# Kernel tuning notes

Hardware: AMD Instinct MI355X
Metric: run time of the kernel (lower is better)

## Reference

```python
import jax, jax.numpy as jnp
import numpy as np
from jax import lax

# Static problem configuration (SAModule(ratio=0.25, r=0.2, MLP([35,64,64,128])))
B, N, C_IN = 8, 4096, 32
RATIO, R, K = 0.25, 0.2, 64   # K == max_num_neighbors
M = int(N * RATIO)            # centroids per cloud after FPS
NEG = -1e10


def setup_inputs() -> dict:
    key = jax.random.key(0)
    ks = jax.random.split(key, 6)
    x = jax.random.normal(ks[0], (B * N, C_IN), jnp.float32)
    pos = jax.random.uniform(ks[1], (B * N, 3), jnp.float32)  # unit cube -> r=0.2 balls are non-trivial
    batch = jnp.repeat(jnp.arange(B, dtype=jnp.int32), N)
    def lin(k, fan_in, fan_out):
        return jax.random.normal(k, (fan_in, fan_out), jnp.float32) * (1.0 / np.sqrt(fan_in))
    W1 = lin(ks[2], C_IN + 3, 64); b1 = jnp.zeros((64,), jnp.float32)
    W2 = lin(ks[3], 64, 64);       b2 = jnp.zeros((64,), jnp.float32)
    W3 = lin(ks[4], 64, 128);      b3 = jnp.zeros((128,), jnp.float32)
    return {"x": x, "pos": pos, "batch": batch,
            "W1": W1, "b1": b1, "W2": W2, "b2": b2, "W3": W3, "b3": b3}


def _fps_one(p):
    """Farthest-point sampling on one cloud p:[N,3] -> idx:[M] (deterministic start at 0)."""
    def body(carry, _):
        dmin, last = carry
        d = jnp.sum((p - p[last]) ** 2, axis=-1)         # [N] sq-dist to last picked point
        dmin = jnp.minimum(dmin, d)
        nxt = jnp.argmax(dmin).astype(jnp.int32)
        return (dmin, nxt), nxt
    init = (jnp.full((N,), 1e10, jnp.float32), jnp.int32(0))
    _, rest = lax.scan(body, init, None, length=M - 1)
    return jnp.concatenate([jnp.zeros((1,), jnp.int32), rest])


def _sa_one(p, xb, ib, W1, b1, W2, b2, W3, b3):
    """Radius ball-query + PointNetConv (gather -> MLP -> masked scatter-max) on one cloud."""
    ctr = p[ib]                                              # [M,3] sampled centroids
    d2 = jnp.sum((ctr[:, None, :] - p[None, :, :]) ** 2, -1)  # [M,N]
    negd, nbr = lax.top_k(-d2, K)                            # K nearest per centroid
    valid = (-negd) <= R * R                                 # inside-ball mask [M,K]
    xj = xb[nbr]                                             # [M,K,C_IN] gathered features
    rel = p[nbr] - ctr[:, None, :]                           # [M,K,3] relative positions
    h = jnp.concatenate([xj, rel], axis=-1)                  # message input [x_j, pos_j - pos_i]
    h = jax.nn.relu(h @ W1 + b1)
    h = jax.nn.relu(h @ W2 + b2)
    h = h @ W3 + b3                                          # plain last layer (PyG MLP plain_last)
    h = jnp.where(valid[..., None], h, NEG)
    return jnp.max(h, axis=1)                                # max aggregation -> [M,128]


def reference(x, pos, batch, W1, b1, W2, b2, W3, b3):
    pos3 = pos.reshape(B, N, 3)
    x3 = x.reshape(B, N, C_IN)
    idx = jax.vmap(_fps_one)(pos3)                           # [B,M]
    conv = lambda p, xb, ib: _sa_one(p, xb, ib, W1, b1, W2, b2, W3, b3)
    x_out = jax.vmap(conv)(pos3, x3, idx)                    # [B,M,128]
    pos_out = jnp.take_along_axis(pos3, idx[..., None], axis=1)  # [B,M,3]
    batch_out = jnp.repeat(jnp.arange(B, dtype=batch.dtype), M)
    return x_out.reshape(B * M, -1), pos_out.reshape(B * M, 3), batch_out
```

## Files before the change

kernel.cpp:

```cpp
#include <hip/hip_runtime.h>
#include <hip/hip_bf16.h>

#define BB 8
#define NN 4096
#define CIN 32
#define MM 1024
#define KNB 64
#define CAND 1024
#define ROWS 72
#define GRID 256
#define NWORK (GRID - 8)

typedef __attribute__((ext_vector_type(8))) short  short8;
typedef __attribute__((ext_vector_type(4))) float  f32x4;
typedef __attribute__((ext_vector_type(2))) float  f32x2;

__device__ __forceinline__ float sq3(float dx, float dy, float dz) {
    return __fadd_rn(__fadd_rn(__fmul_rn(dx, dx), __fmul_rn(dy, dy)), __fmul_rn(dz, dz));
}

__device__ __forceinline__ unsigned short f2bf(float v) {
    union { __hip_bfloat16 b; unsigned short u; } cv;
    cv.b = __float2bfloat16(v);
    return cv.u;
}
__device__ __forceinline__ float bf2f(unsigned short u) {
    union { unsigned short u; __hip_bfloat16 b; } cv;
    cv.u = u;
    return __bfloat162float(cv.b);
}

static __device__ __forceinline__ f32x4 mfma16(short8 a, short8 b, f32x4 c) {
    return __builtin_amdgcn_mfma_f32_16x16x32_bf16(a, b, c, 0, 0, 0);
}

template<int CTRL>
__device__ __forceinline__ unsigned long long dpp_maxkey(unsigned long long k) {
    unsigned int lo = (unsigned int)k;
    unsigned int hi = (unsigned int)(k >> 32);
    unsigned int nlo = (unsigned int)__builtin_amdgcn_update_dpp((int)lo, (int)lo, CTRL, 0xF, 0xF, false);
    unsigned int nhi = (unsigned int)__builtin_amdgcn_update_dpp((int)hi, (int)hi, CTRL, 0xF, 0xF, false);
    unsigned long long nk = ((unsigned long long)nhi << 32) | (unsigned long long)nlo;
    return nk > k ? nk : k;
}

__global__ __launch_bounds__(256) void prep_kernel(
    const float* __restrict__ W1, const float* __restrict__ W2,
    const float* __restrict__ W3, unsigned short* __restrict__ wf)
{
    int gid = blockIdx.x * 256 + threadIdx.x;
    const float* W; int K, Ncol, base, slot;
    if (gid < 1024)      { W = W1; K = 35; Ncol = 64;  base = 0;     slot = gid; }
    else if (gid < 2048) { W = W2; K = 64; Ncol = 64;  base = 8192;  slot = gid - 1024; }
    else                 { W = W3; K = 64; Ncol = 128; base = 16384; slot = gid - 2048; }
    int lane = slot & 63, h = (slot >> 6) & 1, kstep = (slot >> 7) & 1, tile = slot >> 8;
    int col = tile * 16 + (lane & 15), quad = lane >> 4;
#pragma unroll
    for (int j = 0; j < 8; ++j) {
        int k = kstep * 32 + quad * 8 + j;
        float wv = (k < K) ? W[k * Ncol + col] : 0.0f;
        unsigned short hi = f2bf(wv);
        unsigned short v = h ? f2bf(wv - bf2f(hi)) : hi;
        wf[base + slot * 8 + j] = v;
    }
}

struct SaShared {
    unsigned short HA[2 * 64 * ROWS];
    unsigned long long candk[CAND];
    int   cnt;
    int   ok;
    int   sel[KNB];
    float red[4][128];
};

__device__ __forceinline__ void sa_process(
    SaShared& sh, const float* __restrict__ x, const float* __restrict__ P,
    const unsigned short* __restrict__ wf,
    const float* __restrict__ b1, const float* __restrict__ b2,
    const float* __restrict__ b3, float* __restrict__ out, int bm, int b, int ci)
{
    const int t    = threadIdx.x;
    const int w    = t >> 6;
    const int lane = t & 63;
    const float R2 = (float)(0.2 * 0.2);

    if (t == 0) sh.cnt = 0;
    __syncthreads();

    const float cx = P[3 * ci], cy = P[3 * ci + 1], cz = P[3 * ci + 2];

    for (int i = t; i < NN; i += 256) {
        float dx = P[3 * i] - cx, dy = P[3 * i + 1] - cy, dz = P[3 * i + 2] - cz;
        float d2 = sq3(dx, dy, dz);
        bool hit = d2 <= R2;
        unsigned long long mk = __ballot(hit);
        if (mk) {
            int leader = __ffsll((unsigned long long)mk) - 1;
            int base = 0;
            if (lane == leader) base = atomicAdd(&sh.cnt, __popcll(mk));
            base = __shfl(base, leader);
            if (hit) {
                int p = base + __popcll(mk & ((1ull << lane) - 1));
                if (p < CAND)
                    sh.candk[p] = ((unsigned long long)__float_as_uint(d2) << 32)
                                | (unsigned int)i;
            }
        }
    }
    __syncthreads();
    const int n = min(sh.cnt, CAND);
    const int V = min(n, KNB);

    for (int i = t; i < n; i += 256) {
        unsigned long long ki = sh.candk[i];
        int rank = 0;
        for (int j = 0; j < n; ++j)
            rank += (sh.candk[j] < ki) ? 1 : 0;
        if (rank < KNB) sh.sel[rank] = (int)(ki & 0xffffffffu);
    }
    __syncthreads();

    {
        const int row = 16 * w + (lane & 15);
        const int prt = lane >> 4;
        short8 z = {};
        *(short8*)(sh.HA + row * ROWS + 32 + prt * 8) = z;
        *(short8*)(sh.HA + 64 * ROWS + row * ROWS + 32 + prt * 8) = z;
        if (row < V) {
            int g = b * NN + sh.sel[row];
            const float4* xr = (const float4*)(x + (size_t)g * CIN + prt * 8);
            float4 v0 = xr[0], v1 = xr[1];
            float vv[8] = {v0.x, v0.y, v0.z, v0.w, v1.x, v1.y, v1.z, v1.w};
            short8 hv, lv;
#pragma unroll
            for (int j = 0; j < 8; ++j) {
                unsigned short h = f2bf(vv[j]);
                hv[j] = (short)h;
                lv[j] = (short)f2bf(vv[j] - bf2f(h));
            }
            *(short8*)(sh.HA + row * ROWS + prt * 8) = hv;
            *(short8*)(sh.HA + 64 * ROWS + row * ROWS + prt * 8) = lv;
            if (prt == 0) {
                int g2 = sh.sel[row];
#pragma unroll
                for (int c = 0; c < 3; ++c) {
                    float cc = (c == 0) ? cx : (c == 1) ? cy : cz;
                    float rv = P[3 * g2 + c] - cc;
                    unsigned short h = f2bf(rv);
                    sh.HA[row * ROWS + 32 + c] = h;
                    sh.HA[64 * ROWS + row * ROWS + 32 + c] = f2bf(rv - bf2f(h));
                }
            }
        }
    }

    const int m16  = lane & 15;
    const int quad = lane >> 4;
    const int arow = 16 * w + m16;
    const short8* wf8 = (const short8*)wf;

    {
        short8 aH[2], aL[2];
        aH[0] = *(const short8*)(sh.HA + arow * ROWS + quad * 8);
        aH[1] = *(const short8*)(sh.HA + arow * ROWS + 32 + quad * 8);
        aL[0] = *(const short8*)(sh.HA + 64 * ROWS + arow * ROWS + quad * 8);
        aL[1] = *(const short8*)(sh.HA + 64 * ROWS + arow * ROWS + 32 + quad * 8);
#pragma unroll
        for (int tile = 0; tile < 4; ++tile) {
            f32x4 acc = {};
#pragma unroll
            for (int ks = 0; ks < 2; ++ks) {
                short8 bH = wf8[((tile * 2 + ks) * 2 + 0) * 64 + lane];
                short8 bL = wf8[((tile * 2 + ks) * 2 + 1) * 64 + lane];
                acc = mfma16(aH[ks], bH, acc);
                acc = mfma16(aH[ks], bL, acc);
                acc = mfma16(aL[ks], bH, acc);
            }
            int col = tile * 16 + m16;
            float bb = b1[col];
#pragma unroll
            for (int i = 0; i < 4; ++i) {
                int grow = 16 * w + quad * 4 + i;
                float v = fmaxf(acc[i] + bb, 0.0f);
                unsigned short h = f2bf(v);
                sh.HA[grow * ROWS + col] = h;
                sh.HA[64 * ROWS + grow * ROWS + col] = f2bf(v - bf2f(h));
            }
        }
    }

    {
        short8 aH[2], aL[2];
        aH[0] = *(const short8*)(sh.HA + arow * ROWS + quad * 8);
        aH[1] = *(const short8*)(sh.HA + arow * ROWS + 32 + quad * 8);
        aL[0] = *(const short8*)(sh.HA + 64 * ROWS + arow * ROWS + quad * 8);
        aL[1] = *(const short8*)(sh.HA + 64 * ROWS + arow * ROWS + 32 + quad * 8);
#pragma unroll
        for (int tile = 0; tile < 4; ++tile) {
            f32x4 acc = {};
#pragma unroll
            for (int ks = 0; ks < 2; ++ks) {
                short8 bH = wf8[1024 + ((tile * 2 + ks) * 2 + 0) * 64 + lane];
                short8 bL = wf8[1024 + ((tile * 2 + ks) * 2 + 1) * 64 + lane];
                acc = mfma16(aH[ks], bH, acc);
                acc = mfma16(aH[ks], bL, acc);
                acc = mfma16(aL[ks], bH, acc);
            }
            int col = tile * 16 + m16;
            float bb = b2[col];
#pragma unroll
            for (int i = 0; i < 4; ++i) {
                int grow = 16 * w + quad * 4 + i;
                float v = fmaxf(acc[i] + bb, 0.0f);
                unsigned short h = f2bf(v);
                sh.HA[grow * ROWS + col] = h;
                sh.HA[64 * ROWS + grow * ROWS + col] = f2bf(v - bf2f(h));
            }
        }
    }

    {
        short8 aH[2], aL[2];
        aH[0] = *(const short8*)(sh.HA + arow * ROWS + quad * 8);
        aH[1] = *(const short8*)(sh.HA + arow * ROWS + 32 + quad * 8);
        aL[0] = *(const short8*)(sh.HA + 64 * ROWS + arow * ROWS + quad * 8);
        aL[1] = *(const short8*)(sh.HA + 64 * ROWS + arow * ROWS + 32 + quad * 8);
#pragma unroll
        for (int tile = 0; tile < 8; ++tile) {
            f32x4 acc = {};
#pragma unroll
            for (int ks = 0; ks < 2; ++ks) {
                short8 bH = wf8[2048 + ((tile * 2 + ks) * 2 + 0) * 64 + lane];
                short8 bL = wf8[2048 + ((tile * 2 + ks) * 2 + 1) * 64 + lane];
                acc = mfma16(aH[ks], bH, acc);
                acc = mfma16(aH[ks], bL, acc);
                acc = mfma16(aL[ks], bH, acc);
            }
            float mv = -1e10f;
#pragma unroll
            for (int i = 0; i < 4; ++i) {
                int grow = 16 * w + quad * 4 + i;
                float v = (grow < V) ? acc[i] : -1e10f;
                mv = fmaxf(mv, v);
            }
            mv = fmaxf(mv, __shfl_xor(mv, 16));
            mv = fmaxf(mv, __shfl_xor(mv, 32));
            if (lane < 16) sh.red[w][tile * 16 + lane] = mv;
        }
    }
    __syncthreads();

    if (t < 128) {
        float v = fmaxf(fmaxf(sh.red[0][t], sh.red[1][t]),
                        fmaxf(sh.red[2][t], sh.red[3][t]));
        out[(size_t)bm * 128 + t] = v + b3[t];
    }
}

union SharedMem {
    struct {
        float4 plds4[NN];
        int    chosen[MM];
        __align__(16) unsigned long long part[2][4];
    } fps;
    SaShared sa;
};

__global__ __launch_bounds__(256, 2) void fused_kernel(
    const float* __restrict__ x, const float* __restrict__ pos,
    int* __restrict__ idx_ws, unsigned int* __restrict__ ready,
    int* __restrict__ done, const unsigned short* __restrict__ wf,
    const float* __restrict__ b1, const float* __restrict__ b2,
    const float* __restrict__ b3, float* __restrict__ out)
{
    __shared__ SharedMem sh;
    const int t = threadIdx.x;

    if (blockIdx.x < BB) {
        __builtin_amdgcn_s_setprio(3);
        const int b = blockIdx.x;
        const float* P = pos + (size_t)b * NN * 3;
        for (int i = t; i < NN; i += 256) {
            float4 v;
            v.x = P[3 * i]; v.y = P[3 * i + 1]; v.z = P[3 * i + 2]; v.w = 0.0f;
            sh.fps.plds4[i] = v;
        }
        if (t == 0) {
            sh.fps.chosen[0] = 0;
            __hip_atomic_store(&idx_ws[b * MM], 0, __ATOMIC_RELAXED,
                               __HIP_MEMORY_SCOPE_AGENT);
        }
        __syncthreads();

        f32x2 pxv[8], pyv[8], pzv[8], dminv[8];
#pragma unroll
        for (int s = 0; s < 8; ++s) {
            float4 a = sh.fps.plds4[t + 512 * s];
            float4 c = sh.fps.plds4[t + 512 * s + 256];
            pxv[s] = (f32x2){a.x, c.x};
            pyv[s] = (f32x2){a.y, c.y};
            pzv[s] = (f32x2){a.z, c.z};
            dminv[s] = (f32x2){1e10f, 1e10f};
        }

        int win = 0;
        for (int it = 1; it < MM; ++it) {
            float4 wc = sh.fps.plds4[win];
            const f32x2 lxv = (f32x2){wc.x, wc.x};
            const f32x2 lyv = (f32x2){wc.y, wc.y};
            const f32x2 lzv = (f32x2){wc.z, wc.z};
            float bv = -1.0f;
            int   bi = 0;
#pragma unroll
            for (int s = 0; s < 8; ++s) {
                f32x2 d;
                {
#pragma clang fp contract(off)
                    f32x2 dx = pxv[s] - lxv;
                    f32x2 dy = pyv[s] - lyv;
                    f32x2 dz = pzv[s] - lzv;
                    d = dx * dx + dy * dy + dz * dz;
                }
                float m0 = fminf(dminv[s].x, d.x);
                float m1 = fminf(dminv[s].y, d.y);
                dminv[s].x = m0;
                dminv[s].y = m1;
                if (m0 > bv) { bv = m0; bi = t + 512 * s; }
                if (m1 > bv) { bv = m1; bi = t + 512 * s + 256; }
            }
            unsigned long long k =
                ((unsigned long long)__float_as_uint(bv) << 32) | (unsigned int)(~bi);
            k = dpp_maxkey<0x111>(k);
            k = dpp_maxkey<0x112>(k);
            k = dpp_maxkey<0x114>(k);
            k = dpp_maxkey<0x118>(k);
            k = dpp_maxkey<0x142>(k);
            k = dpp_maxkey<0x143>(k);
            if ((t & 63) == 63) sh.fps.part[it & 1][t >> 6] = k;
            __syncthreads();
            const ulonglong2* pp = (const ulonglong2*)&sh.fps.part[it & 1][0];
            ulonglong2 p01 = pp[0], p23 = pp[1];
            unsigned long long ka = p01.x > p01.y ? p01.x : p01.y;
            unsigned long long kb = p23.x > p23.y ? p23.x : p23.y;
            unsigned long long km = ka > kb ? ka : kb;
            win = (int)(~(unsigned int)km);
            if (t == 0) {
                sh.fps.chosen[it] = win;
                __hip_atomic_store(&idx_ws[b * MM + it], win, __ATOMIC_RELAXED,
                                   __HIP_MEMORY_SCOPE_AGENT);
                if ((it & 31) == 31)
                    __hip_atomic_store(&ready[b], (unsigned int)(it + 1),
                                       __ATOMIC_RELEASE, __HIP_MEMORY_SCOPE_AGENT);
            }
        }
        __syncthreads();

        for (int m = t; m < MM; m += 256) {
            int mi = sh.fps.chosen[m];
            const int PO = BB * MM * 128;
            const int BO = PO + BB * MM * 3;
            int row = b * MM + m;
            float4 c = sh.fps.plds4[mi];
            out[PO + 3 * row + 0] = c.x;
            out[PO + 3 * row + 1] = c.y;
            out[PO + 3 * row + 2] = c.z;
            out[BO + row] = (float)b;
        }
        return;
    }

    int budget = 8000;
    for (int item = (int)blockIdx.x - BB; item < BB * MM; item += NWORK) {
        const int m  = item >> 3;
        const int b  = item & 7;
        const int bm = b * MM + m;
        const float* P = pos + (size_t)b * NN * 3;

        if (t == 0) {
            const unsigned int need = (unsigned int)(m + 1);
            while (budget > 0 &&
                   __hip_atomic_load(&ready[b], __ATOMIC_ACQUIRE,
                                     __HIP_MEMORY_SCOPE_AGENT) < need) {
                __builtin_amdgcn_s_sleep(10);
                --budget;
            }
            sh.sa.ok = (__hip_atomic_load(&ready[b], __ATOMIC_ACQUIRE,
                                          __HIP_MEMORY_SCOPE_AGENT) >= need) ? 1 : 0;
        }
        __syncthreads();
        const int myok = sh.sa.ok;
        __syncthreads();
        if (!myok) continue;

        const int ci = __hip_atomic_load(&idx_ws[bm], __ATOMIC_RELAXED,
                                         __HIP_MEMORY_SCOPE_AGENT) & (NN - 1);
        sa_process(sh.sa, x, P, wf, b1, b2, b3, out, bm, b, ci);
        if (t == 0)
            __hip_atomic_store(&done[bm], 1, __ATOMIC_RELAXED,
                               __HIP_MEMORY_SCOPE_AGENT);
    }
}

__global__ __launch_bounds__(256, 4) void sweep_kernel(
    const float* __restrict__ x, const float* __restrict__ pos,
    const int* __restrict__ idx_ws, const int* __restrict__ done,
    const unsigned short* __restrict__ wf,
    const float* __restrict__ b1, const float* __restrict__ b2,
    const float* __restrict__ b3, float* __restrict__ out)
{
    __shared__ SaShared sh;
    const int bm = blockIdx.x;
    if (done[bm]) return;
    const int b = bm >> 10;
    const float* P = pos + (size_t)b * NN * 3;
    const int ci = idx_ws[bm] & (NN - 1);
    sa_process(sh, x, P, wf, b1, b2, b3, out, bm, b, ci);
}

extern "C" void kernel_launch(void* const* d_in, const int* in_sizes, int n_in,
                              void* d_out, int out_size, void* d_ws, size_t ws_size,
                              hipStream_t stream) {
    const float* x   = (const float*)d_in[0];
    const float* pos = (const float*)d_in[1];
    const float* W1 = (const float*)d_in[3];
    const float* b1 = (const float*)d_in[4];
    const float* W2 = (const float*)d_in[5];
    const float* b2 = (const float*)d_in[6];
    const float* W3 = (const float*)d_in[7];
    const float* b3 = (const float*)d_in[8];
    float* out    = (float*)d_out;
    int*   idx_ws = (int*)d_ws;
    unsigned short* wf = (unsigned short*)((char*)d_ws + 32768);
    unsigned int* ready = (unsigned int*)((char*)d_ws + 98304);
    int* done = (int*)((char*)d_ws + 98368);

    hipMemsetAsync((char*)d_ws + 98304, 0, 131136 - 98304, stream);
    hipLaunchKernelGGL(prep_kernel, dim3(16), dim3(256), 0, stream, W1, W2, W3, wf);
    hipLaunchKernelGGL(fused_kernel, dim3(GRID), dim3(256), 0, stream,
                       x, pos, idx_ws, ready, done, wf, b1, b2, b3, out);
    hipLaunchKernelGGL(sweep_kernel, dim3(BB * MM), dim3(256), 0, stream,
                       x, pos, idx_ws, done, wf, b1, b2, b3, out);
}
```

Before: 707.9 us.

## Force one block per CU and rewrite FPS inner loop with packed math

Pads shared memory and sets launch bounds to one block per CU so the FPS blocks never share a compute unit with SA worker blocks, and drops the priority boost. Rewrites the FPS distance update with explicit v_pk_add/v_pk_mul packed instructions and separates the max search from the index recovery, which shortens the per-iteration dependency chain. The ready flag is now published every 64 iterations instead of 32. In exchange, worker occupancy halves and consumers see new centroids in coarser batches.

```diff
diff --git a/kernel.cpp b/kernel.cpp
--- a/kernel.cpp
+++ b/kernel.cpp
@@ -17,6 +17,13 @@
 
 __device__ __forceinline__ float sq3(float dx, float dy, float dz) {
     return __fadd_rn(__fadd_rn(__fmul_rn(dx, dx), __fmul_rn(dy, dy)), __fmul_rn(dz, dz));
+}
+
+__device__ __forceinline__ f32x2 pk_add(f32x2 a, f32x2 b) {
+    f32x2 d; asm("v_pk_add_f32 %0, %1, %2" : "=v"(d) : "v"(a), "v"(b)); return d;
+}
+__device__ __forceinline__ f32x2 pk_mul(f32x2 a, f32x2 b) {
+    f32x2 d; asm("v_pk_mul_f32 %0, %1, %2" : "=v"(d) : "v"(a), "v"(b)); return d;
 }
 
 __device__ __forceinline__ unsigned short f2bf(float v) {
@@ -265,9 +272,10 @@
         __align__(16) unsigned long long part[2][4];
     } fps;
     SaShared sa;
+    char occupancy_pad[86016];
 };
 
-__global__ __launch_bounds__(256, 2) void fused_kernel(
+__global__ __launch_bounds__(256, 1) void fused_kernel(
     const float* __restrict__ x, const float* __restrict__ pos,
     int* __restrict__ idx_ws, unsigned int* __restrict__ ready,
     int* __restrict__ done, const unsigned short* __restrict__ wf,
@@ -278,7 +286,6 @@
     const int t = threadIdx.x;
 
     if (blockIdx.x < BB) {
-        __builtin_amdgcn_s_setprio(3);
         const int b = blockIdx.x;
         const float* P = pos + (size_t)b * NN * 3;
         for (int i = t; i < NN; i += 256) {
@@ -307,27 +314,32 @@
         int win = 0;
         for (int it = 1; it < MM; ++it) {
             float4 wc = sh.fps.plds4[win];
-            const f32x2 lxv = (f32x2){wc.x, wc.x};
-            const f32x2 lyv = (f32x2){wc.y, wc.y};
-            const f32x2 lzv = (f32x2){wc.z, wc.z};
-            float bv = -1.0f;
-            int   bi = 0;
+            const f32x2 lxn = (f32x2){-wc.x, -wc.x};
+            const f32x2 lyn = (f32x2){-wc.y, -wc.y};
+            const f32x2 lzn = (f32x2){-wc.z, -wc.z};
+            float bv0 = -1.0f, bv1 = -1.0f;
 #pragma unroll
             for (int s = 0; s < 8; ++s) {
-                f32x2 d;
-                {
-#pragma clang fp contract(off)
-                    f32x2 dx = pxv[s] - lxv;
-                    f32x2 dy = pyv[s] - lyv;
-                    f32x2 dz = pzv[s] - lzv;
-                    d = dx * dx + dy * dy + dz * dz;
-                }
-                float m0 = fminf(dminv[s].x, d.x);
-                float m1 = fminf(dminv[s].y, d.y);
-                dminv[s].x = m0;
-                dminv[s].y = m1;
-                if (m0 > bv) { bv = m0; bi = t + 512 * s; }
-                if (m1 > bv) { bv = m1; bi = t + 512 * s + 256; }
+                f32x2 dx = pk_add(pxv[s], lxn);
+                f32x2 dy = pk_add(pyv[s], lyn);
+                f32x2 dz = pk_add(pzv[s], lzn);
+                f32x2 t1 = pk_mul(dx, dx);
+                f32x2 t2 = pk_mul(dy, dy);
+                f32x2 t3 = pk_mul(dz, dz);
+                f32x2 d  = pk_add(pk_add(t1, t2), t3);
+                f32x2 dm;
+                dm.x = fminf(dminv[s].x, d.x);
+                dm.y = fminf(dminv[s].y, d.y);
+                dminv[s] = dm;
+                bv0 = fmaxf(bv0, dm.x);
+                bv1 = fmaxf(bv1, dm.y);
+            }
+            const float bv = fmaxf(bv0, bv1);
+            int bi = 0;
+#pragma unroll
+            for (int s = 7; s >= 0; --s) {
+                if (dminv[s].y == bv) bi = t + 512 * s + 256;
+                if (dminv[s].x == bv) bi = t + 512 * s;
             }
             unsigned long long k =
                 ((unsigned long long)__float_as_uint(bv) << 32) | (unsigned int)(~bi);
@@ -349,7 +361,7 @@
                 sh.fps.chosen[it] = win;
                 __hip_atomic_store(&idx_ws[b * MM + it], win, __ATOMIC_RELAXED,
                                    __HIP_MEMORY_SCOPE_AGENT);
-                if ((it & 31) == 31)
+                if ((it & 63) == 63)
                     __hip_atomic_store(&ready[b], (unsigned int)(it + 1),
                                        __ATOMIC_RELEASE, __HIP_MEMORY_SCOPE_AGENT);
             }
```

After: 796.3 us. 1.12x slower.

## Carry winner coordinates through FPS reduction and force one block per CU

Applied to the files above, without the earlier changes.

In the FPS loop, each lane now tracks the coordinates of its best point, and the winning lane of each wave writes them to LDS along with its key. This removes the dependent LDS load of the winner's position at the start of the next iteration. Shared memory is padded and launch bounds are lowered to one block per CU, probably so the FPS blocks get a CU to themselves. The s_setprio call is removed. The cost is lower occupancy for the SA worker blocks, plus extra registers and selects in the FPS loop.

```diff
diff --git a/kernel.cpp b/kernel.cpp
--- a/kernel.cpp
+++ b/kernel.cpp
@@ -262,12 +262,16 @@
     struct {
         float4 plds4[NN];
         int    chosen[MM];
-        __align__(16) unsigned long long part[2][4];
+        __align__(16) unsigned long long partK[2][4];
+        __align__(16) float partX[2][4];
+        __align__(16) float partY[2][4];
+        __align__(16) float partZ[2][4];
     } fps;
     SaShared sa;
+    char occupancy_pad[86016];
 };
 
-__global__ __launch_bounds__(256, 2) void fused_kernel(
+__global__ __launch_bounds__(256, 1) void fused_kernel(
     const float* __restrict__ x, const float* __restrict__ pos,
     int* __restrict__ idx_ws, unsigned int* __restrict__ ready,
     int* __restrict__ done, const unsigned short* __restrict__ wf,
@@ -278,7 +282,6 @@
     const int t = threadIdx.x;
 
     if (blockIdx.x < BB) {
-        __builtin_amdgcn_s_setprio(3);
         const int b = blockIdx.x;
         const float* P = pos + (size_t)b * NN * 3;
         for (int i = t; i < NN; i += 256) {
@@ -304,14 +307,17 @@
             dminv[s] = (f32x2){1e10f, 1e10f};
         }
 
-        int win = 0;
+        float wx, wy, wz;
+        { float4 c0 = sh.fps.plds4[0]; wx = c0.x; wy = c0.y; wz = c0.z; }
+
         for (int it = 1; it < MM; ++it) {
-            float4 wc = sh.fps.plds4[win];
-            const f32x2 lxv = (f32x2){wc.x, wc.x};
-            const f32x2 lyv = (f32x2){wc.y, wc.y};
-            const f32x2 lzv = (f32x2){wc.z, wc.z};
+            const int par = it & 1;
+            const f32x2 lxv = (f32x2){wx, wx};
+            const f32x2 lyv = (f32x2){wy, wy};
+            const f32x2 lzv = (f32x2){wz, wz};
             float bv = -1.0f;
             int   bi = 0;
+            float bx = 0.0f, by = 0.0f, bz = 0.0f;
 #pragma unroll
             for (int s = 0; s < 8; ++s) {
                 f32x2 d;
@@ -326,25 +332,43 @@
                 float m1 = fminf(dminv[s].y, d.y);
                 dminv[s].x = m0;
                 dminv[s].y = m1;
-                if (m0 > bv) { bv = m0; bi = t + 512 * s; }
-                if (m1 > bv) { bv = m1; bi = t + 512 * s + 256; }
-            }
-            unsigned long long k =
+                if (m0 > bv) { bv = m0; bi = t + 512 * s;
+                               bx = pxv[s].x; by = pyv[s].x; bz = pzv[s].x; }
+                if (m1 > bv) { bv = m1; bi = t + 512 * s + 256;
+                               bx = pxv[s].y; by = pyv[s].y; bz = pzv[s].y; }
+            }
+            unsigned long long k0 =
                 ((unsigned long long)__float_as_uint(bv) << 32) | (unsigned int)(~bi);
+            unsigned long long k = k0;
             k = dpp_maxkey<0x111>(k);
             k = dpp_maxkey<0x112>(k);
             k = dpp_maxkey<0x114>(k);
             k = dpp_maxkey<0x118>(k);
             k = dpp_maxkey<0x142>(k);
             k = dpp_maxkey<0x143>(k);
-            if ((t & 63) == 63) sh.fps.part[it & 1][t >> 6] = k;
+            unsigned int kl = (unsigned int)__builtin_amdgcn_readlane((int)(unsigned int)k, 63);
+            unsigned int kh = (unsigned int)__builtin_amdgcn_readlane((int)(unsigned int)(k >> 32), 63);
+            unsigned long long kmax = ((unsigned long long)kh << 32) | kl;
+            if (k0 == kmax) {
+                const int w4 = t >> 6;
+                sh.fps.partK[par][w4] = k0;
+                sh.fps.partX[par][w4] = bx;
+                sh.fps.partY[par][w4] = by;
+                sh.fps.partZ[par][w4] = bz;
+            }
             __syncthreads();
-            const ulonglong2* pp = (const ulonglong2*)&sh.fps.part[it & 1][0];
-            ulonglong2 p01 = pp[0], p23 = pp[1];
-            unsigned long long ka = p01.x > p01.y ? p01.x : p01.y;
-            unsigned long long kb = p23.x > p23.y ? p23.x : p23.y;
+            ulonglong2 k01 = *(const ulonglong2*)&sh.fps.partK[par][0];
+            ulonglong2 k23 = *(const ulonglong2*)&sh.fps.partK[par][2];
+            float4 fx = *(const float4*)&sh.fps.partX[par][0];
+            float4 fy = *(const float4*)&sh.fps.partY[par][0];
+            float4 fz = *(const float4*)&sh.fps.partZ[par][0];
+            unsigned long long ka = k01.x > k01.y ? k01.x : k01.y;
+            unsigned long long kb = k23.x > k23.y ? k23.x : k23.y;
             unsigned long long km = ka > kb ? ka : kb;
-            win = (int)(~(unsigned int)km);
+            wx = (k01.x == km) ? fx.x : (k01.y == km) ? fx.y : (k23.x == km) ? fx.z : fx.w;
+            wy = (k01.x == km) ? fy.x : (k01.y == km) ? fy.y : (k23.x == km) ? fy.z : fy.w;
+            wz = (k01.x == km) ? fz.x : (k01.y == km) ? fz.y : (k23.x == km) ? fz.z : fz.w;
+            const int win = (int)(~(unsigned int)km);
             if (t == 0) {
                 sh.fps.chosen[it] = win;
                 __hip_atomic_store(&idx_ws[b * MM + it], win, __ATOMIC_RELAXED,
```

After: 1.151 ms. 1.63x slower.
